# Kernel optimization log

Hardware: AMD Instinct MI355X
Metric: run time of the kernel (lower is better)

The kernel has to match this reference:

```python
import jax, jax.numpy as jnp
import numpy as np

EPS = 1e-7  # K.epsilon()

def squash(v, axis=-1):
    sn = jnp.sum(jnp.square(v), axis=axis, keepdims=True)
    scale = sn / (1.0 + sn) / jnp.sqrt(sn + EPS)
    return scale * v

def setup_inputs() -> dict:
    key = jax.random.key(0)
    k1, k2, k3 = jax.random.split(key, 3)
    B, In, Din = 32, 2048, 8
    N, Dout, C = 64, 16, 32
    x = jax.random.normal(k1, (B, In, Din), dtype=jnp.float32)
    W = jax.random.normal(k2, (N, C, Dout, Din), dtype=jnp.float32) * 0.1
    B_bias = jax.random.normal(k3, (N, Dout), dtype=jnp.float32) * 0.1
    return {"x": x, "W": W, "B_bias": B_bias}

def reference(x, W, B_bias):
    routings = 3
    N, C, Dout, Din = W.shape
    In = x.shape[1]
    # repeat channel weights to cover all input capsules: [N, In, Dout, Din]
    W2 = jnp.repeat(W, In // C, axis=1)
    # vote vectors: inputs_hat[b,n,i,d] = sum_k x[b,i,k] * W2[n,i,d,k]
    inputs_hat = jnp.einsum('bik,nidk->bnid', x, W2)  # [B, N, In, Dout]
    b = jnp.zeros(inputs_hat.shape[:3], dtype=inputs_hat.dtype)  # [B, N, In]
    outputs = None
    for i in range(routings):
        c = jax.nn.softmax(b, axis=1)  # softmax over num_capsule axis
        s = jnp.einsum('bni,bnid->bnd', c, inputs_hat) + B_bias
        outputs = squash(s)
        if i < routings - 1:
            b = b + jnp.einsum('bnd,bnid->bni', outputs, inputs_hat)
    return outputs
```

## Files before the change

kernel.cpp:

```cpp
#include <hip/hip_runtime.h>
#include <math.h>

constexpr int B_    = 32;
constexpr int In_   = 2048;
constexpr int Din_  = 8;
constexpr int N_    = 64;
constexpr int Dout_ = 16;
constexpr int C_    = 32;
constexpr int ICP   = 64;
constexpr float EPS = 1e-7f;

__global__ __launch_bounds__(256) void caps_pre(
    const float* __restrict__ x, const float* __restrict__ W,
    const float* __restrict__ bias, float* __restrict__ v0)
{
    const int b = blockIdx.x, t = threadIdx.x;

    __shared__ float xs[In_ * Din_];
    __shared__ float xbar[C_][Din_];
    __shared__ float s0[N_][Dout_ + 1];
    __shared__ float scl[N_];

    const float4* xg = (const float4*)(x + (size_t)b * In_ * Din_);
    #pragma unroll
    for (int q = 0; q < 16; ++q) ((float4*)xs)[t + 256 * q] = xg[t + 256 * q];
    __syncthreads();

    {
        const int c = t >> 3, k = t & 7;
        float acc = 0.f;
        #pragma unroll
        for (int ii = 0; ii < ICP; ++ii) {
            const int i = (ii + c) & 63;
            acc += xs[(c * ICP + i) * Din_ + k];
        }
        xbar[c][k] = acc * (1.f / 64.f);
    }
    __syncthreads();

    {
        float acc[4]; int nn[4], dd[4];
        #pragma unroll
        for (int q = 0; q < 4; ++q) {
            const int it = t + 256 * q;
            nn[q] = it >> 4; dd[q] = it & 15;
            acc[q] = bias[nn[q] * Dout_ + dd[q]];
        }
        for (int c = 0; c < C_; ++c) {
            float xb[8];
            #pragma unroll
            for (int k = 0; k < 8; ++k) xb[k] = xbar[c][k];
            #pragma unroll
            for (int q = 0; q < 4; ++q) {
                const float4* wp = (const float4*)(W + ((nn[q] * C_ + c) * Dout_ + dd[q]) * Din_);
                const float4 w0 = wp[0], w1 = wp[1];
                acc[q] += w0.x * xb[0] + w0.y * xb[1] + w0.z * xb[2] + w0.w * xb[3]
                        + w1.x * xb[4] + w1.y * xb[5] + w1.z * xb[6] + w1.w * xb[7];
            }
        }
        #pragma unroll
        for (int q = 0; q < 4; ++q) s0[nn[q]][dd[q]] = acc[q];
    }
    __syncthreads();

    if (t < N_) {
        float sn = 0.f;
        #pragma unroll
        for (int d = 0; d < Dout_; ++d) sn += s0[t][d] * s0[t][d];
        scl[t] = sn / (1.f + sn) / sqrtf(sn + EPS);
    }
    __syncthreads();

    {
        const int n = t >> 2, d0 = (t & 3) * 4;
        const float sc = scl[n];
        float4 o;
        o.x = s0[n][d0 + 0] * sc; o.y = s0[n][d0 + 1] * sc;
        o.z = s0[n][d0 + 2] * sc; o.w = s0[n][d0 + 3] * sc;
        ((float4*)(v0 + (size_t)b * N_ * Dout_))[t] = o;
    }
}

__global__ __launch_bounds__(256) void caps_route(
    const float* __restrict__ x, const float* __restrict__ W,
    const float* __restrict__ bias, const float* __restrict__ v_src,
    const float* __restrict__ s_src, float* __restrict__ U_g,
    float* __restrict__ s_out, int accumulate)
{
    const int b = blockIdx.x >> 5;
    const int c = blockIdx.x & 31;
    const int t = threadIdx.x;
    const int w = t >> 6, l = t & 63;
    const int n4 = t >> 2, q4 = t & 3;

    __shared__ float vs[N_][20];
    __shared__ float Us[N_][8];
    __shared__ float xs[ICP][8];
    __shared__ float lg[ICP][68];
    __shared__ float ps[4][ICP];
    __shared__ float inv_s[ICP];
    __shared__ float ys[4][N_][8];

    {
        float4 a;
        if (s_src) {
            a = *(const float4*)(bias + n4 * 16 + q4 * 4);
            for (int cc = 0; cc < 32; ++cc) {
                const float4 p = *(const float4*)(s_src + (((size_t)b * 32 + cc) * 64 + n4) * 16 + q4 * 4);
                a.x += p.x; a.y += p.y; a.z += p.z; a.w += p.w;
            }
            float sn = a.x * a.x + a.y * a.y + a.z * a.z + a.w * a.w;
            sn += __shfl_xor(sn, 1);
            sn += __shfl_xor(sn, 2);
            const float sc = sn / (1.f + sn) / sqrtf(sn + EPS);
            a.x *= sc; a.y *= sc; a.z *= sc; a.w *= sc;
        } else {
            a = *(const float4*)(v_src + ((size_t)b * 64 + n4) * 16 + q4 * 4);
        }
        *(float4*)&vs[n4][q4 * 4] = a;
    }
    __syncthreads();

    {
        float pU[8] = {0, 0, 0, 0, 0, 0, 0, 0};
        #pragma unroll
        for (int dd = 0; dd < 4; ++dd) {
            const int d = q4 * 4 + dd;
            const float4* wp = (const float4*)(W + (((size_t)n4 * 32 + c) * 16 + d) * 8);
            const float4 w0 = wp[0], w1 = wp[1];
            const float vd = vs[n4][d];
            pU[0] += vd * w0.x; pU[1] += vd * w0.y; pU[2] += vd * w0.z; pU[3] += vd * w0.w;
            pU[4] += vd * w1.x; pU[5] += vd * w1.y; pU[6] += vd * w1.z; pU[7] += vd * w1.w;
        }
        #pragma unroll
        for (int k = 0; k < 8; ++k) {
            pU[k] += __shfl_xor(pU[k], 1);
            pU[k] += __shfl_xor(pU[k], 2);
        }
        float2 u2;
        u2.x = pU[2 * q4]; u2.y = pU[2 * q4 + 1];
        float2* ug = (float2*)(U_g + (((size_t)b * 32 + c) * 64 + n4) * 8 + 2 * q4);
        if (accumulate) {
            const float2 o = *ug;
            u2.x += o.x; u2.y += o.y;
        } else {
            *ug = u2;
        }
        *(float2*)&Us[n4][2 * q4] = u2;
    }

    float xr[8];
    {
        const float4* xp = (const float4*)(x + ((size_t)b * In_ + c * ICP + l) * 8);
        const float4 x0 = xp[0], x1 = xp[1];
        xr[0] = x0.x; xr[1] = x0.y; xr[2] = x0.z; xr[3] = x0.w;
        xr[4] = x1.x; xr[5] = x1.y; xr[6] = x1.z; xr[7] = x1.w;
        if (w == 0) {
            *(float4*)&xs[l][0] = x0;
            *(float4*)&xs[l][4] = x1;
        }
    }
    __syncthreads();

    {
        float e[16];
        float ssum = 0.f;
        #pragma unroll
        for (int nn = 0; nn < 16; ++nn) {
            const int n = w * 16 + nn;
            const float4 u0 = *(const float4*)&Us[n][0];
            const float4 u1 = *(const float4*)&Us[n][4];
            float a = u0.x * xr[0] + u0.y * xr[1] + u0.z * xr[2] + u0.w * xr[3]
                    + u1.x * xr[4] + u1.y * xr[5] + u1.z * xr[6] + u1.w * xr[7];
            const float ee = __expf(a);
            e[nn] = ee; ssum += ee;
        }
        #pragma unroll
        for (int qq = 0; qq < 4; ++qq) {
            float4 o;
            o.x = e[qq * 4 + 0]; o.y = e[qq * 4 + 1]; o.z = e[qq * 4 + 2]; o.w = e[qq * 4 + 3];
            *(float4*)&lg[l][w * 16 + qq * 4] = o;
        }
        ps[w][l] = ssum;
    }
    __syncthreads();

    if (t < 64) inv_s[t] = 1.f / (ps[0][t] + ps[1][t] + ps[2][t] + ps[3][t]);
    __syncthreads();

    {
        const int nq = l >> 2, kq = l & 3;
        float y[8] = {0, 0, 0, 0, 0, 0, 0, 0};
        #pragma unroll
        for (int ii = 0; ii < 16; ++ii) {
            const int i = w * 16 + ii;
            const float4 cw = *(const float4*)&lg[i][nq * 4];
            const float iv = inv_s[i];
            const float2 x2 = *(const float2*)&xs[i][kq * 2];
            const float c0 = cw.x * iv, c1 = cw.y * iv, c2 = cw.z * iv, c3 = cw.w * iv;
            y[0] += c0 * x2.x; y[1] += c0 * x2.y;
            y[2] += c1 * x2.x; y[3] += c1 * x2.y;
            y[4] += c2 * x2.x; y[5] += c2 * x2.y;
            y[6] += c3 * x2.x; y[7] += c3 * x2.y;
        }
        #pragma unroll
        for (int j = 0; j < 4; ++j) {
            float2 o; o.x = y[2 * j]; o.y = y[2 * j + 1];
            *(float2*)&ys[w][nq * 4 + j][kq * 2] = o;
        }
    }
    __syncthreads();

    {
        float yn[8];
        #pragma unroll
        for (int k = 0; k < 8; ++k)
            yn[k] = ys[0][n4][k] + ys[1][n4][k] + ys[2][n4][k] + ys[3][n4][k];
        float4 o;
        float* op = (float*)&o;
        #pragma unroll
        for (int dd = 0; dd < 4; ++dd) {
            const int d = q4 * 4 + dd;
            const float4* wp = (const float4*)(W + (((size_t)n4 * 32 + c) * 16 + d) * 8);
            const float4 w0 = wp[0], w1 = wp[1];
            op[dd] = w0.x * yn[0] + w0.y * yn[1] + w0.z * yn[2] + w0.w * yn[3]
                   + w1.x * yn[4] + w1.y * yn[5] + w1.z * yn[6] + w1.w * yn[7];
        }
        *(float4*)(s_out + (((size_t)b * 32 + c) * 64 + n4) * 16 + q4 * 4) = o;
    }
}

__global__ __launch_bounds__(256) void caps_out(
    const float* __restrict__ s_src, const float* __restrict__ bias,
    float* __restrict__ out)
{
    const int b = blockIdx.x, t = threadIdx.x;
    const int n = t >> 2, q = t & 3;

    float4 a = *(const float4*)(bias + n * 16 + q * 4);
    for (int cc = 0; cc < 32; ++cc) {
        const float4 p = *(const float4*)(s_src + (((size_t)b * 32 + cc) * 64 + n) * 16 + q * 4);
        a.x += p.x; a.y += p.y; a.z += p.z; a.w += p.w;
    }
    float sn = a.x * a.x + a.y * a.y + a.z * a.z + a.w * a.w;
    sn += __shfl_xor(sn, 1);
    sn += __shfl_xor(sn, 2);
    const float sc = sn / (1.f + sn) / sqrtf(sn + EPS);
    float4 o;
    o.x = a.x * sc; o.y = a.y * sc; o.z = a.z * sc; o.w = a.w * sc;
    *(float4*)(out + (size_t)b * 1024 + t * 4) = o;
}

extern "C" void kernel_launch(void* const* d_in, const int* in_sizes, int n_in,
                              void* d_out, int out_size, void* d_ws, size_t ws_size,
                              hipStream_t stream) {
    const float* x    = (const float*)d_in[0];
    const float* W    = (const float*)d_in[1];
    const float* bias = (const float*)d_in[2];
    float* out = (float*)d_out;

    float* ws  = (float*)d_ws;
    float* s1  = ws;
    float* s2  = s1  + (size_t)B_ * C_ * N_ * Dout_;
    float* U_g = s2  + (size_t)B_ * C_ * N_ * Dout_;
    float* v0  = U_g + (size_t)B_ * C_ * N_ * Din_;

    caps_pre  <<<B_,      256, 0, stream>>>(x, W, bias, v0);
    caps_route<<<B_ * C_, 256, 0, stream>>>(x, W, bias, v0, nullptr, U_g, s1, 0);
    caps_route<<<B_ * C_, 256, 0, stream>>>(x, W, bias, nullptr, s1, U_g, s2, 1);
    caps_out  <<<B_,      256, 0, stream>>>(s2, bias, out);
}
```

Baseline: 108.2 us.

## Split prologue and reductions across more blocks, replace U accumulation with v-sum

The prologue now runs as 256 blocks, each computing 8 output capsules, instead of 32 blocks that each staged the whole x batch in shared memory. The cross-channel reduction and squash that every route block repeated is moved into a separate, widely parallel reduce kernel. That kernel also adds v0 so the second routing pass uses v0+v1 directly, which drops the global U_g buffer and its read-modify-write. The cost is one extra kernel launch in exchange for removing 32x redundant reduction work and raising parallelism in the small kernels.

After: 90.56 us. -16.3%, faster.

```diff
diff --git a/kernel.cpp b/kernel.cpp
--- a/kernel.cpp
+++ b/kernel.cpp
@@ -10,82 +10,55 @@
 constexpr int ICP   = 64;
 constexpr float EPS = 1e-7f;
 
-__global__ __launch_bounds__(256) void caps_pre(
+__global__ __launch_bounds__(256) void caps_v0(
     const float* __restrict__ x, const float* __restrict__ W,
     const float* __restrict__ bias, float* __restrict__ v0)
 {
-    const int b = blockIdx.x, t = threadIdx.x;
-
-    __shared__ float xs[In_ * Din_];
+    const int b = blockIdx.x >> 3, j = blockIdx.x & 7;
+    const int t = threadIdx.x;
+
     __shared__ float xbar[C_][Din_];
-    __shared__ float s0[N_][Dout_ + 1];
-    __shared__ float scl[N_];
-
-    const float4* xg = (const float4*)(x + (size_t)b * In_ * Din_);
-    #pragma unroll
-    for (int q = 0; q < 16; ++q) ((float4*)xs)[t + 256 * q] = xg[t + 256 * q];
-    __syncthreads();
 
     {
         const int c = t >> 3, k = t & 7;
+        const float* xp = x + (size_t)b * In_ * Din_ + (size_t)c * ICP * Din_ + k;
         float acc = 0.f;
-        #pragma unroll
-        for (int ii = 0; ii < ICP; ++ii) {
-            const int i = (ii + c) & 63;
-            acc += xs[(c * ICP + i) * Din_ + k];
-        }
+        #pragma unroll 8
+        for (int i = 0; i < ICP; ++i) acc += xp[i * Din_];
         xbar[c][k] = acc * (1.f / 64.f);
     }
     __syncthreads();
 
     {
-        float acc[4]; int nn[4], dd[4];
-        #pragma unroll
-        for (int q = 0; q < 4; ++q) {
-            const int it = t + 256 * q;
-            nn[q] = it >> 4; dd[q] = it & 15;
-            acc[q] = bias[nn[q] * Dout_ + dd[q]];
-        }
-        for (int c = 0; c < C_; ++c) {
-            float xb[8];
-            #pragma unroll
-            for (int k = 0; k < 8; ++k) xb[k] = xbar[c][k];
-            #pragma unroll
-            for (int q = 0; q < 4; ++q) {
-                const float4* wp = (const float4*)(W + ((nn[q] * C_ + c) * Dout_ + dd[q]) * Din_);
-                const float4 w0 = wp[0], w1 = wp[1];
-                acc[q] += w0.x * xb[0] + w0.y * xb[1] + w0.z * xb[2] + w0.w * xb[3]
-                        + w1.x * xb[4] + w1.y * xb[5] + w1.z * xb[6] + w1.w * xb[7];
-            }
-        }
-        #pragma unroll
-        for (int q = 0; q < 4; ++q) s0[nn[q]][dd[q]] = acc[q];
-    }
-    __syncthreads();
-
-    if (t < N_) {
-        float sn = 0.f;
-        #pragma unroll
-        for (int d = 0; d < Dout_; ++d) sn += s0[t][d] * s0[t][d];
-        scl[t] = sn / (1.f + sn) / sqrtf(sn + EPS);
-    }
-    __syncthreads();
-
-    {
-        const int n = t >> 2, d0 = (t & 3) * 4;
-        const float sc = scl[n];
-        float4 o;
-        o.x = s0[n][d0 + 0] * sc; o.y = s0[n][d0 + 1] * sc;
-        o.z = s0[n][d0 + 2] * sc; o.w = s0[n][d0 + 3] * sc;
-        ((float4*)(v0 + (size_t)b * N_ * Dout_))[t] = o;
+        const int nl = t >> 5, lane32 = t & 31;
+        const int d = lane32 >> 1, h = lane32 & 1;
+        const int n = j * 8 + nl;
+
+        float a = 0.f;
+        #pragma unroll
+        for (int cc = 0; cc < 16; ++cc) {
+            const int c2 = cc * 2 + h;
+            const float4* wp = (const float4*)(W + (((size_t)n * C_ + c2) * Dout_ + d) * Din_);
+            const float4 w0 = wp[0], w1 = wp[1];
+            a += w0.x * xbar[c2][0] + w0.y * xbar[c2][1] + w0.z * xbar[c2][2] + w0.w * xbar[c2][3]
+               + w1.x * xbar[c2][4] + w1.y * xbar[c2][5] + w1.z * xbar[c2][6] + w1.w * xbar[c2][7];
+        }
+        a += __shfl_xor(a, 1);
+        a += bias[n * Dout_ + d];
+
+        float sn = a * a;
+        sn += __shfl_xor(sn, 2);
+        sn += __shfl_xor(sn, 4);
+        sn += __shfl_xor(sn, 8);
+        sn += __shfl_xor(sn, 16);
+        const float sc = sn / (1.f + sn) / sqrtf(sn + EPS);
+        if (h == 0) v0[(size_t)b * 1024 + n * Dout_ + d] = a * sc;
     }
 }
 
 __global__ __launch_bounds__(256) void caps_route(
     const float* __restrict__ x, const float* __restrict__ W,
-    const float* __restrict__ bias, const float* __restrict__ v_src,
-    const float* __restrict__ s_src, float* __restrict__ U_g,
-    float* __restrict__ s_out, int accumulate)
+    const float* __restrict__ v_src, float* __restrict__ s_out)
 {
     const int b = blockIdx.x >> 5;
     const int c = blockIdx.x & 31;
@@ -93,7 +66,6 @@
     const int w = t >> 6, l = t & 63;
     const int n4 = t >> 2, q4 = t & 3;
 
-    __shared__ float vs[N_][20];
     __shared__ float Us[N_][8];
     __shared__ float xs[ICP][8];
     __shared__ float lg[ICP][68];
@@ -102,50 +74,24 @@
     __shared__ float ys[4][N_][8];
 
     {
-        float4 a;
-        if (s_src) {
-            a = *(const float4*)(bias + n4 * 16 + q4 * 4);
-            for (int cc = 0; cc < 32; ++cc) {
-                const float4 p = *(const float4*)(s_src + (((size_t)b * 32 + cc) * 64 + n4) * 16 + q4 * 4);
-                a.x += p.x; a.y += p.y; a.z += p.z; a.w += p.w;
-            }
-            float sn = a.x * a.x + a.y * a.y + a.z * a.z + a.w * a.w;
-            sn += __shfl_xor(sn, 1);
-            sn += __shfl_xor(sn, 2);
-            const float sc = sn / (1.f + sn) / sqrtf(sn + EPS);
-            a.x *= sc; a.y *= sc; a.z *= sc; a.w *= sc;
-        } else {
-            a = *(const float4*)(v_src + ((size_t)b * 64 + n4) * 16 + q4 * 4);
-        }
-        *(float4*)&vs[n4][q4 * 4] = a;
-    }
-    __syncthreads();
-
-    {
+        const float4 vv = *(const float4*)(v_src + ((size_t)b * 64 + n4) * 16 + q4 * 4);
+        const float vd[4] = {vv.x, vv.y, vv.z, vv.w};
         float pU[8] = {0, 0, 0, 0, 0, 0, 0, 0};
         #pragma unroll
         for (int dd = 0; dd < 4; ++dd) {
             const int d = q4 * 4 + dd;
             const float4* wp = (const float4*)(W + (((size_t)n4 * 32 + c) * 16 + d) * 8);
             const float4 w0 = wp[0], w1 = wp[1];
-            const float vd = vs[n4][d];
-            pU[0] += vd * w0.x; pU[1] += vd * w0.y; pU[2] += vd * w0.z; pU[3] += vd * w0.w;
-            pU[4] += vd * w1.x; pU[5] += vd * w1.y; pU[6] += vd * w1.z; pU[7] += vd * w1.w;
+            const float v_ = vd[dd];
+            pU[0] += v_ * w0.x; pU[1] += v_ * w0.y; pU[2] += v_ * w0.z; pU[3] += v_ * w0.w;
+            pU[4] += v_ * w1.x; pU[5] += v_ * w1.y; pU[6] += v_ * w1.z; pU[7] += v_ * w1.w;
         }
         #pragma unroll
         for (int k = 0; k < 8; ++k) {
             pU[k] += __shfl_xor(pU[k], 1);
             pU[k] += __shfl_xor(pU[k], 2);
         }
-        float2 u2;
-        u2.x = pU[2 * q4]; u2.y = pU[2 * q4 + 1];
-        float2* ug = (float2*)(U_g + (((size_t)b * 32 + c) * 64 + n4) * 8 + 2 * q4);
-        if (accumulate) {
-            const float2 o = *ug;
-            u2.x += o.x; u2.y += o.y;
-        } else {
-            *ug = u2;
-        }
+        float2 u2; u2.x = pU[2 * q4]; u2.y = pU[2 * q4 + 1];
         *(float2*)&Us[n4][2 * q4] = u2;
     }
 
@@ -155,10 +101,7 @@
         const float4 x0 = xp[0], x1 = xp[1];
         xr[0] = x0.x; xr[1] = x0.y; xr[2] = x0.z; xr[3] = x0.w;
         xr[4] = x1.x; xr[5] = x1.y; xr[6] = x1.z; xr[7] = x1.w;
-        if (w == 0) {
-            *(float4*)&xs[l][0] = x0;
-            *(float4*)&xs[l][4] = x1;
-        }
+        if (w == 0) { *(float4*)&xs[l][0] = x0; *(float4*)&xs[l][4] = x1; }
     }
     __syncthreads();
 
@@ -170,8 +113,8 @@
             const int n = w * 16 + nn;
             const float4 u0 = *(const float4*)&Us[n][0];
             const float4 u1 = *(const float4*)&Us[n][4];
-            float a = u0.x * xr[0] + u0.y * xr[1] + u0.z * xr[2] + u0.w * xr[3]
-                    + u1.x * xr[4] + u1.y * xr[5] + u1.z * xr[6] + u1.w * xr[7];
+            const float a = u0.x * xr[0] + u0.y * xr[1] + u0.z * xr[2] + u0.w * xr[3]
+                          + u1.x * xr[4] + u1.y * xr[5] + u1.z * xr[6] + u1.w * xr[7];
             const float ee = __expf(a);
             e[nn] = ee; ssum += ee;
         }
@@ -204,9 +147,9 @@
             y[6] += c3 * x2.x; y[7] += c3 * x2.y;
         }
         #pragma unroll
-        for (int j = 0; j < 4; ++j) {
-            float2 o; o.x = y[2 * j]; o.y = y[2 * j + 1];
-            *(float2*)&ys[w][nq * 4 + j][kq * 2] = o;
+        for (int jj = 0; jj < 4; ++jj) {
+            float2 o; o.x = y[2 * jj]; o.y = y[2 * jj + 1];
+            *(float2*)&ys[w][nq * 4 + jj][kq * 2] = o;
         }
     }
     __syncthreads();
@@ -230,25 +173,34 @@
     }
 }
 
-__global__ __launch_bounds__(256) void caps_out(
+__global__ __launch_bounds__(256) void caps_reduce(
     const float* __restrict__ s_src, const float* __restrict__ bias,
-    float* __restrict__ out)
+    const float* __restrict__ vadd, float* __restrict__ dst)
 {
-    const int b = blockIdx.x, t = threadIdx.x;
-    const int n = t >> 2, q = t & 3;
-
-    float4 a = *(const float4*)(bias + n * 16 + q * 4);
-    for (int cc = 0; cc < 32; ++cc) {
-        const float4 p = *(const float4*)(s_src + (((size_t)b * 32 + cc) * 64 + n) * 16 + q * 4);
-        a.x += p.x; a.y += p.y; a.z += p.z; a.w += p.w;
-    }
-    float sn = a.x * a.x + a.y * a.y + a.z * a.z + a.w * a.w;
-    sn += __shfl_xor(sn, 1);
+    const int b = blockIdx.x >> 3, j = blockIdx.x & 7;
+    const int t = threadIdx.x;
+    const int nl = t >> 5, lane32 = t & 31;
+    const int d = lane32 >> 1, h = lane32 & 1;
+    const int n = j * 8 + nl;
+
+    float a = 0.f;
+    #pragma unroll
+    for (int cc = 0; cc < 16; ++cc) {
+        const int c2 = cc * 2 + h;
+        a += s_src[(((size_t)b * 32 + c2) * 64 + n) * 16 + d];
+    }
+    a += __shfl_xor(a, 1);
+    a += bias[n * Dout_ + d];
+
+    float sn = a * a;
     sn += __shfl_xor(sn, 2);
+    sn += __shfl_xor(sn, 4);
+    sn += __shfl_xor(sn, 8);
+    sn += __shfl_xor(sn, 16);
     const float sc = sn / (1.f + sn) / sqrtf(sn + EPS);
-    float4 o;
-    o.x = a.x * sc; o.y = a.y * sc; o.z = a.z * sc; o.w = a.w * sc;
-    *(float4*)(out + (size_t)b * 1024 + t * 4) = o;
+    float val = a * sc;
+    if (vadd) val += vadd[(size_t)b * 1024 + n * Dout_ + d];
+    if (h == 0) dst[(size_t)b * 1024 + n * Dout_ + d] = val;
 }
 
 extern "C" void kernel_launch(void* const* d_in, const int* in_sizes, int n_in,
@@ -259,14 +211,15 @@
     const float* bias = (const float*)d_in[2];
     float* out = (float*)d_out;
 
-    float* ws  = (float*)d_ws;
-    float* s1  = ws;
-    float* s2  = s1  + (size_t)B_ * C_ * N_ * Dout_;
-    float* U_g = s2  + (size_t)B_ * C_ * N_ * Dout_;
-    float* v0  = U_g + (size_t)B_ * C_ * N_ * Din_;
-
-    caps_pre  <<<B_,      256, 0, stream>>>(x, W, bias, v0);
-    caps_route<<<B_ * C_, 256, 0, stream>>>(x, W, bias, v0, nullptr, U_g, s1, 0);
-    caps_route<<<B_ * C_, 256, 0, stream>>>(x, W, bias, nullptr, s1, U_g, s2, 1);
-    caps_out  <<<B_,      256, 0, stream>>>(s2, bias, out);
-}
+    float* ws   = (float*)d_ws;
+    float* s1   = ws;
+    float* s2   = s1   + (size_t)B_ * C_ * N_ * Dout_;
+    float* v0   = s2   + (size_t)B_ * C_ * N_ * Dout_;
+    float* vsum = v0   + (size_t)B_ * N_ * Dout_;
+
+    caps_v0    <<<256,  256, 0, stream>>>(x, W, bias, v0);
+    caps_route <<<1024, 256, 0, stream>>>(x, W, v0, s1);
+    caps_reduce<<<256,  256, 0, stream>>>(s1, bias, v0, vsum);
+    caps_route <<<1024, 256, 0, stream>>>(x, W, vsum, s2);
+    caps_reduce<<<256,  256, 0, stream>>>(s2, bias, nullptr, out);
+}
```
